# Kernel optimization log

Measured on AMD Instinct MI355X. Metric: run time of the kernel, lower is better.

The kernel has to match this reference:

```python
import jax, jax.numpy as jnp
import numpy as np

SEQ, NSTEPS = 8192, 2048
IDIM, HDIM, NL = 256, 1024, 4


def setup_inputs() -> dict:
    key = jax.random.key(0)
    ks = jax.random.split(key, 6)
    s = 0.02  # small init so tanh recurrence stays well-conditioned
    return {
        "xs": jax.random.normal(ks[0], (SEQ, IDIM), dtype=jnp.float32),
        "Wx0": jax.random.normal(ks[1], (IDIM, HDIM), dtype=jnp.float32) * s,
        "Wh0": jax.random.normal(ks[2], (HDIM, HDIM), dtype=jnp.float32) * s,
        "b0": jnp.zeros((HDIM,), dtype=jnp.float32),
        "Wx_rest": jax.random.normal(ks[3], (NL - 1, HDIM, HDIM), dtype=jnp.float32) * s,
        "Wh_rest": jax.random.normal(ks[4], (NL - 1, HDIM, HDIM), dtype=jnp.float32) * s,
        "b_rest": jnp.zeros((NL - 1, HDIM), dtype=jnp.float32),
        "out_W": jax.random.normal(ks[5], (IDIM, HDIM), dtype=jnp.float32) * s,  # eqx Linear: (out, in)
        "out_b": jnp.zeros((IDIM,), dtype=jnp.float32),
        "n_steps": NSTEPS,
    }


def _layer_scan(xs, Wx, Wh, b):
    # open-loop scan of one tanh RNN cell over the whole sequence
    pre = xs @ Wx + b  # (T, H): hoist input projection out of the scan

    def step(h, p):
        h = jnp.tanh(p + h @ Wh)
        return h, h

    h0 = jnp.zeros((Wh.shape[0],), dtype=xs.dtype)
    last, outs = jax.lax.scan(step, h0, pre)
    return last, outs


def reference(xs, Wx0, Wh0, b0, Wx_rest, Wh_rest, b_rest, out_W, out_b, n_steps):
    # open_loop: run each layer's scan over the full sequence
    states = []
    h, seq = _layer_scan(xs, Wx0, Wh0, b0)
    states.append(h)
    for i in range(Wx_rest.shape[0]):
        h, seq = _layer_scan(seq, Wx_rest[i], Wh_rest[i], b_rest[i])
        states.append(h)
    ol_outs = seq @ out_W.T + out_b  # (T, IDIM) vmap'd out_layer

    def ar_step(carry, _):
        sts, x = carry
        new_sts = []
        h = jnp.tanh(x @ Wx0 + sts[0] @ Wh0 + b0)
        new_sts.append(h)
        x = h
        for i in range(Wx_rest.shape[0]):
            h = jnp.tanh(x @ Wx_rest[i] + sts[i + 1] @ Wh_rest[i] + b_rest[i])
            new_sts.append(h)
            x = h
        x = out_W @ x + out_b
        return (tuple(new_sts), x), x

    carry = (tuple(states), ol_outs[-1])
    _, ar_outs = jax.lax.scan(ar_step, carry, None, length=n_steps)
    return jnp.concatenate([ol_outs, ar_outs], axis=0)  # (T + n_steps, IDIM)
```

## Files before the change

### kernel.cpp

```cpp
#include <hip/hip_runtime.h>
#include <math.h>

#define SEQ    8192
#define NSTEPS 2048
#define NTOT   (SEQ + NSTEPS)
#define IDIM   256
#define HDIM   1024

#define NWG    128
#define TPB    512
#define WPB    8
#define RD     32
#define CREDIT (RD - 8)

typedef unsigned long long u64;

#define WT_FLOATS   (8ull*HDIM*HDIM)
#define BF_FLOAT    WT_FLOATS
#define RING_FLOAT  (WT_FLOATS + HDIM)
#define RING_U64S   (4ull*RD*HDIM)
#define PROG_FLOAT  (RING_FLOAT + 2ull*RING_U64S)


__global__ void k_fuse_w(const float* __restrict__ outW, const float* __restrict__ Wx0,
                         float* __restrict__ ws) {
    int l = blockIdx.x * 256 + threadIdx.x;
    int j = blockIdx.y;
    float acc = 0.f;
    for (int k = 0; k < IDIM; ++k)
        acc += outW[(size_t)k * HDIM + l] * Wx0[(size_t)k * HDIM + j];
    ws[(size_t)j * HDIM + l] = acc;
}

__global__ void k_fuse_b(const float* __restrict__ b0, const float* __restrict__ outb,
                         const float* __restrict__ Wx0, float* __restrict__ ws) {
    int j = blockIdx.x * 256 + threadIdx.x;
    float acc = b0[j];
    for (int k = 0; k < IDIM; ++k)
        acc += outb[k] * Wx0[(size_t)k * HDIM + j];
    ws[BF_FLOAT + j] = acc;
}

__global__ void k_pack(const float* __restrict__ Wh0, const float* __restrict__ Wxr,
                       const float* __restrict__ Whr, float* __restrict__ ws) {
    __shared__ float t[32][33];
    int z = blockIdx.z;
    const float* src; int slot;
    if (z == 0)      { src = Wh0;                                  slot = 1; }
    else if (z <= 3) { src = Wxr + (size_t)(z - 1) * HDIM * HDIM;  slot = 2 * z; }
    else             { src = Whr + (size_t)(z - 4) * HDIM * HDIM;  slot = 2 * (z - 4) + 3; }
    int j0 = blockIdx.x * 32, l0 = blockIdx.y * 32;
    t[threadIdx.y][threadIdx.x] = src[(size_t)(l0 + threadIdx.y) * HDIM + j0 + threadIdx.x];
    __syncthreads();
    float* dst = ws + (size_t)slot * HDIM * HDIM;
    dst[(size_t)(j0 + threadIdx.y) * HDIM + (l0 + threadIdx.x)] = t[threadIdx.x][threadIdx.y];
}

__global__ void k_init(float* __restrict__ ws) {
    int t = blockIdx.x * blockDim.x + threadIdx.x;
    ((u64*)(ws + RING_FLOAT))[t] = 0ull;
    if (t < NWG) ((unsigned*)(ws + PROG_FLOAT))[t] = 0u;
}


__device__ __forceinline__ float wsum(float v) {
#pragma unroll
    for (int off = 32; off > 0; off >>= 1) v += __shfl_xor(v, off, 64);
    return v;
}

__device__ __forceinline__ int wmin(int v) {
#pragma unroll
    for (int off = 32; off > 0; off >>= 1) {
        int o = __shfl_xor(v, off, 64);
        v = o < v ? o : v;
    }
    return v;
}

__device__ __forceinline__ float ftanh(float x) {
    x = fminf(15.f, fmaxf(-15.f, x));
    float e = __builtin_amdgcn_exp2f(x * 2.8853900817779268f);
    return (e - 1.f) * __builtin_amdgcn_rcpf(e + 1.f);
}

__device__ __forceinline__ void capture8(const u64* slot, unsigned want,
                                         float* dst, int lane, int kbase) {
    unsigned done = 0;
    for (;;) {
        u64 v[8];
#pragma unroll
        for (int k = 0; k < 8; ++k) {
            v[k] = 0;
            if (!(done & (1u << k)))
                v[k] = __hip_atomic_load(slot + lane + 64 * (kbase + k),
                                         __ATOMIC_RELAXED, __HIP_MEMORY_SCOPE_AGENT);
        }
#pragma unroll
        for (int k = 0; k < 8; ++k) {
            if (!(done & (1u << k)) && ((unsigned)(v[k] >> 32) == want)) {
                dst[lane + 64 * (kbase + k)] = __uint_as_float((unsigned)v[k]);
                done |= 1u << k;
            }
        }
        if (__all(done == 0xFFu)) return;
    }
}

__global__ __launch_bounds__(TPB, 1) void k_scan(
    const float* __restrict__ xs, const float* __restrict__ Wx0,
    const float* __restrict__ b0, const float* __restrict__ brest,
    const float* __restrict__ outW, const float* __restrict__ outb,
    float* __restrict__ ws, float* __restrict__ out)
{
    const int lane  = threadIdx.x & 63;
    const int wv    = threadIdx.x >> 6;
    const int layer = blockIdx.x >> 5;
    const int wgl   = blockIdx.x & 31;
    const int jw    = wgl * WPB + wv;
    const int j0    = jw * 4;

    __shared__ float ldsOwn[2][HDIM];
    __shared__ float ldsUp[2][HDIM];
    __shared__ int   ldsMinp;

    u64* ring = (u64*)(ws + RING_FLOAT);
    unsigned* prog = (unsigned*)(ws + PROG_FLOAT);
    const int cons = (layer + 1) & 3;

    if (threadIdx.x == 0) ldsMinp = 0;

    float A[4][16], B[4][16];
#pragma unroll
    for (int c = 0; c < 4; ++c)
#pragma unroll
        for (int k = 0; k < 16; ++k) {
            A[c][k] = ws[((size_t)(2 * layer) * HDIM + (j0 + c)) * HDIM + lane + 64 * k];
            B[c][k] = ws[((size_t)(2 * layer + 1) * HDIM + (j0 + c)) * HDIM + lane + 64 * k];
        }
    float wx0[4][4];
    if (layer == 0) {
#pragma unroll
        for (int c = 0; c < 4; ++c)
#pragma unroll
            for (int k = 0; k < 4; ++k)
                wx0[c][k] = Wx0[(size_t)(lane + 64 * k) * HDIM + (j0 + c)];
    }
    float ow[16]; float obv = 0.f;
    if (layer == 3) {
#pragma unroll
        for (int k = 0; k < 16; ++k) ow[k] = outW[(size_t)jw * HDIM + lane + 64 * k];
        obv = outb[jw];
    }
    float bb[4], bfc[4];
#pragma unroll
    for (int c = 0; c < 4; ++c) {
        bb[c]  = (layer == 0) ? b0[j0 + c] : brest[(size_t)(layer - 1) * HDIM + j0 + c];
        bfc[c] = (layer == 0) ? ws[BF_FLOAT + j0 + c] : 0.f;
    }

    float xv[4] = {0.f, 0.f, 0.f, 0.f}, xp[4] = {0.f, 0.f, 0.f, 0.f};
    if (layer == 0) {
#pragma unroll
        for (int k = 0; k < 4; ++k) xv[k] = xs[lane + 64 * k];
    }

    unsigned pvReg = 0;

    __syncthreads();

    for (int n = 1; n <= NTOT; ++n) {
        const int par = n & 1;
        const bool xphase = (layer == 0) && (n <= SEQ);

        if (wv == 5) {
            int m = wmin((int)pvReg);
            if (lane == 0)
                __hip_atomic_store(&ldsMinp, m, __ATOMIC_RELAXED, __HIP_MEMORY_SCOPE_WORKGROUP);
            while (m < n - CREDIT) {
                __builtin_amdgcn_s_sleep(2);
                unsigned p = __hip_atomic_load(&prog[cons * 32 + (lane & 31)],
                                               __ATOMIC_RELAXED, __HIP_MEMORY_SCOPE_AGENT);
                m = wmin((int)p);
                if (lane == 0)
                    __hip_atomic_store(&ldsMinp, m, __ATOMIC_RELAXED, __HIP_MEMORY_SCOPE_WORKGROUP);
            }
        } else {
            if (__hip_atomic_load(&ldsMinp, __ATOMIC_RELAXED, __HIP_MEMORY_SCOPE_WORKGROUP)
                < n - CREDIT) {
                do { __builtin_amdgcn_s_sleep(2); }
                while (__hip_atomic_load(&ldsMinp, __ATOMIC_RELAXED, __HIP_MEMORY_SCOPE_WORKGROUP)
                       < n - CREDIT);
            }
        }

        if (wv < 2) {
            capture8(ring + ((size_t)layer * RD + ((n - 1) & (RD - 1))) * HDIM,
                     (unsigned)(n - 1), ldsOwn[par], lane, wv * 8);
        } else if (wv < 4 && !xphase) {
            const int ul = (layer == 0) ? 3 : layer - 1;
            const unsigned want = (layer == 0) ? (unsigned)(n - 1) : (unsigned)n;
            capture8(ring + ((size_t)ul * RD + (want & (RD - 1))) * HDIM,
                     want, ldsUp[par], lane, (wv - 2) * 8);
        }
        __syncthreads();
        if (threadIdx.x == 0)
            __hip_atomic_store(&prog[blockIdx.x], (unsigned)n, __ATOMIC_RELAXED, __HIP_MEMORY_SCOPE_AGENT);

        if (xphase && n < SEQ) {
            const float* xr = xs + (size_t)n * IDIM;
#pragma unroll
            for (int k = 0; k < 4; ++k) xp[k] = xr[lane + 64 * k];
        }
        if (wv == 5)
            pvReg = __hip_atomic_load(&prog[cons * 32 + (lane & 31)],
                                      __ATOMIC_RELAXED, __HIP_MEMORY_SCOPE_AGENT);

        float a0 = 0.f, a1 = 0.f, a2 = 0.f, a3 = 0.f;
        if (xphase) {
#pragma unroll
            for (int k = 0; k < 4; ++k) {
                float x = xv[k];
                a0 += x * wx0[0][k]; a1 += x * wx0[1][k]; a2 += x * wx0[2][k]; a3 += x * wx0[3][k];
            }
        } else {
#pragma unroll
            for (int k = 0; k < 16; ++k) {
                float x = ldsUp[par][lane + 64 * k];
                a0 += x * A[0][k]; a1 += x * A[1][k]; a2 += x * A[2][k]; a3 += x * A[3][k];
            }
        }
#pragma unroll
        for (int k = 0; k < 16; ++k) {
            float y = ldsOwn[par][lane + 64 * k];
            a0 += y * B[0][k]; a1 += y * B[1][k]; a2 += y * B[2][k]; a3 += y * B[3][k];
        }
        a0 = wsum(a0); a1 = wsum(a1); a2 = wsum(a2); a3 = wsum(a3);
        const bool fph = (layer == 0) && (n > SEQ);
        float r0 = ftanh(a0 + (fph ? bfc[0] : bb[0]));
        float r1 = ftanh(a1 + (fph ? bfc[1] : bb[1]));
        float r2 = ftanh(a2 + (fph ? bfc[2] : bb[2]));
        float r3 = ftanh(a3 + (fph ? bfc[3] : bb[3]));

        {
            u64* dst = ring + ((size_t)layer * RD + (n & (RD - 1))) * HDIM + j0;
            if (lane < 4) {
                float v = (lane == 0) ? r0 : (lane == 1) ? r1 : (lane == 2) ? r2 : r3;
                __hip_atomic_store(dst + lane,
                                   ((u64)(unsigned)n << 32) | (u64)__float_as_uint(v),
                                   __ATOMIC_RELAXED, __HIP_MEMORY_SCOPE_AGENT);
            }
        }

        if (layer == 3 && n >= 2) {
            float a = 0.f;
#pragma unroll
            for (int k = 0; k < 16; ++k) a += ldsOwn[par][lane + 64 * k] * ow[k];
            a = wsum(a);
            if (lane == 0) out[(size_t)(n - 2) * IDIM + jw] = a + obv;
        }

        if (xphase && n < SEQ) {
#pragma unroll
            for (int k = 0; k < 4; ++k) xv[k] = xp[k];
        }
    }

    if (layer == 3) {
        if (wv < 2)
            capture8(ring + ((size_t)3 * RD + (NTOT & (RD - 1))) * HDIM,
                     (unsigned)NTOT, ldsOwn[0], lane, wv * 8);
        __syncthreads();
        float a = 0.f;
#pragma unroll
        for (int k = 0; k < 16; ++k) a += ldsOwn[0][lane + 64 * k] * ow[k];
        a = wsum(a);
        if (lane == 0) out[(size_t)(NTOT - 1) * IDIM + jw] = a + obv;
    }
}


extern "C" void kernel_launch(void* const* d_in, const int* in_sizes, int n_in,
                              void* d_out, int out_size, void* d_ws, size_t ws_size,
                              hipStream_t stream) {
    (void)in_sizes; (void)n_in; (void)out_size; (void)ws_size;
    const float* xs   = (const float*)d_in[0];
    const float* Wx0  = (const float*)d_in[1];
    const float* Wh0  = (const float*)d_in[2];
    const float* b0   = (const float*)d_in[3];
    const float* Wxr  = (const float*)d_in[4];
    const float* Whr  = (const float*)d_in[5];
    const float* brst = (const float*)d_in[6];
    const float* outW = (const float*)d_in[7];
    const float* outb = (const float*)d_in[8];
    float* ws  = (float*)d_ws;
    float* out = (float*)d_out;

    k_fuse_w<<<dim3(4, HDIM), dim3(256), 0, stream>>>(outW, Wx0, ws);
    k_fuse_b<<<dim3(4), dim3(256), 0, stream>>>(b0, outb, Wx0, ws);
    k_pack<<<dim3(32, 32, 7), dim3(32, 32), 0, stream>>>(Wh0, Wxr, Whr, ws);
    k_init<<<dim3(256), dim3(512), 0, stream>>>(ws);

    void* args[] = { (void*)&xs, (void*)&Wx0, (void*)&b0, (void*)&brst,
                     (void*)&outW, (void*)&outb, (void*)&ws, (void*)&out };
    hipError_t e = hipLaunchCooperativeKernel((void*)k_scan, dim3(NWG), dim3(TPB),
                                              args, 0, stream);
    if (e != hipSuccess) {
        k_scan<<<dim3(NWG), dim3(TPB), 0, stream>>>(xs, Wx0, b0, brst, outW, outb, ws, out);
    }
}
```

Baseline: 50.55 ms.

## Halve waves per workgroup, give each wave 8 rows, per-wave credit polling

Each workgroup now has 4 waves instead of 8, and each wave owns 8 hidden rows instead of 4. That doubles the register-resident weights per wave (256 floats for A and B), and each wave now computes two output rows. The shared-LDS credit broadcast from a dedicated wave is replaced by every wave polling the consumer progress flags itself. The capture loop is double-buffered so the next atomic loads are in flight while the previous batch is checked. The aim is to cut per-step barrier and wave-coordination overhead. The cost is much higher register pressure, with possible spills, and more global polling traffic.

```diff
diff --git a/kernel.cpp b/kernel.cpp
--- a/kernel.cpp
+++ b/kernel.cpp
@@ -8,8 +8,8 @@
 #define HDIM   1024
 
 #define NWG    128
-#define TPB    512
-#define WPB    8
+#define TPB    256
+#define WPB    4
 #define RD     32
 #define CREDIT (RD - 8)
 
@@ -86,20 +86,38 @@
 
 __device__ __forceinline__ void capture8(const u64* slot, unsigned want,
                                          float* dst, int lane, int kbase) {
+    const u64* p = slot + lane + 64 * kbase;
     unsigned done = 0;
+    u64 va[8];
+#pragma unroll
+    for (int k = 0; k < 8; ++k)
+        va[k] = __hip_atomic_load(p + 64 * k, __ATOMIC_RELAXED, __HIP_MEMORY_SCOPE_AGENT);
     for (;;) {
-        u64 v[8];
+        u64 vb[8];
 #pragma unroll
         for (int k = 0; k < 8; ++k) {
-            v[k] = 0;
+            vb[k] = 0;
             if (!(done & (1u << k)))
-                v[k] = __hip_atomic_load(slot + lane + 64 * (kbase + k),
-                                         __ATOMIC_RELAXED, __HIP_MEMORY_SCOPE_AGENT);
+                vb[k] = __hip_atomic_load(p + 64 * k, __ATOMIC_RELAXED, __HIP_MEMORY_SCOPE_AGENT);
         }
 #pragma unroll
         for (int k = 0; k < 8; ++k) {
-            if (!(done & (1u << k)) && ((unsigned)(v[k] >> 32) == want)) {
-                dst[lane + 64 * (kbase + k)] = __uint_as_float((unsigned)v[k]);
+            if (!(done & (1u << k)) && ((unsigned)(va[k] >> 32) == want)) {
+                dst[lane + 64 * (kbase + k)] = __uint_as_float((unsigned)va[k]);
+                done |= 1u << k;
+            }
+        }
+        if (__all(done == 0xFFu)) return;
+#pragma unroll
+        for (int k = 0; k < 8; ++k) {
+            va[k] = 0;
+            if (!(done & (1u << k)))
+                va[k] = __hip_atomic_load(p + 64 * k, __ATOMIC_RELAXED, __HIP_MEMORY_SCOPE_AGENT);
+        }
+#pragma unroll
+        for (int k = 0; k < 8; ++k) {
+            if (!(done & (1u << k)) && ((unsigned)(vb[k] >> 32) == want)) {
+                dst[lane + 64 * (kbase + k)] = __uint_as_float((unsigned)vb[k]);
                 done |= 1u << k;
             }
         }
@@ -118,43 +136,43 @@
     const int layer = blockIdx.x >> 5;
     const int wgl   = blockIdx.x & 31;
     const int jw    = wgl * WPB + wv;
-    const int j0    = jw * 4;
+    const int j0    = jw * 8;
 
     __shared__ float ldsOwn[2][HDIM];
     __shared__ float ldsUp[2][HDIM];
-    __shared__ int   ldsMinp;
 
     u64* ring = (u64*)(ws + RING_FLOAT);
     unsigned* prog = (unsigned*)(ws + PROG_FLOAT);
     const int cons = (layer + 1) & 3;
 
-    if (threadIdx.x == 0) ldsMinp = 0;
-
-    float A[4][16], B[4][16];
-#pragma unroll
-    for (int c = 0; c < 4; ++c)
+    float A[8][16], B[8][16];
+#pragma unroll
+    for (int c = 0; c < 8; ++c)
 #pragma unroll
         for (int k = 0; k < 16; ++k) {
             A[c][k] = ws[((size_t)(2 * layer) * HDIM + (j0 + c)) * HDIM + lane + 64 * k];
             B[c][k] = ws[((size_t)(2 * layer + 1) * HDIM + (j0 + c)) * HDIM + lane + 64 * k];
         }
-    float wx0[4][4];
+    float wx0[8][4];
     if (layer == 0) {
 #pragma unroll
-        for (int c = 0; c < 4; ++c)
+        for (int c = 0; c < 8; ++c)
 #pragma unroll
             for (int k = 0; k < 4; ++k)
                 wx0[c][k] = Wx0[(size_t)(lane + 64 * k) * HDIM + (j0 + c)];
     }
-    float ow[16]; float obv = 0.f;
+    float ow0[16], ow1[16]; float ob0 = 0.f, ob1 = 0.f;
     if (layer == 3) {
 #pragma unroll
-        for (int k = 0; k < 16; ++k) ow[k] = outW[(size_t)jw * HDIM + lane + 64 * k];
-        obv = outb[jw];
-    }
-    float bb[4], bfc[4];
-#pragma unroll
-    for (int c = 0; c < 4; ++c) {
+        for (int k = 0; k < 16; ++k) {
+            ow0[k] = outW[(size_t)(2 * jw)     * HDIM + lane + 64 * k];
+            ow1[k] = outW[(size_t)(2 * jw + 1) * HDIM + lane + 64 * k];
+        }
+        ob0 = outb[2 * jw]; ob1 = outb[2 * jw + 1];
+    }
+    float bb[8], bfc[8];
+#pragma unroll
+    for (int c = 0; c < 8; ++c) {
         bb[c]  = (layer == 0) ? b0[j0 + c] : brest[(size_t)(layer - 1) * HDIM + j0 + c];
         bfc[c] = (layer == 0) ? ws[BF_FLOAT + j0 + c] : 0.f;
     }
@@ -165,39 +183,26 @@
         for (int k = 0; k < 4; ++k) xv[k] = xs[lane + 64 * k];
     }
 
-    unsigned pvReg = 0;
-
-    __syncthreads();
+    int minp = 0;
 
     for (int n = 1; n <= NTOT; ++n) {
         const int par = n & 1;
         const bool xphase = (layer == 0) && (n <= SEQ);
 
-        if (wv == 5) {
-            int m = wmin((int)pvReg);
-            if (lane == 0)
-                __hip_atomic_store(&ldsMinp, m, __ATOMIC_RELAXED, __HIP_MEMORY_SCOPE_WORKGROUP);
-            while (m < n - CREDIT) {
+        if (minp < n - CREDIT) {
+            for (;;) {
+                unsigned pv = __hip_atomic_load(&prog[cons * 32 + (lane & 31)],
+                                                __ATOMIC_RELAXED, __HIP_MEMORY_SCOPE_AGENT);
+                minp = wmin((int)pv);
+                if (minp >= n - CREDIT) break;
                 __builtin_amdgcn_s_sleep(2);
-                unsigned p = __hip_atomic_load(&prog[cons * 32 + (lane & 31)],
-                                               __ATOMIC_RELAXED, __HIP_MEMORY_SCOPE_AGENT);
-                m = wmin((int)p);
-                if (lane == 0)
-                    __hip_atomic_store(&ldsMinp, m, __ATOMIC_RELAXED, __HIP_MEMORY_SCOPE_WORKGROUP);
-            }
-        } else {
-            if (__hip_atomic_load(&ldsMinp, __ATOMIC_RELAXED, __HIP_MEMORY_SCOPE_WORKGROUP)
-                < n - CREDIT) {
-                do { __builtin_amdgcn_s_sleep(2); }
-                while (__hip_atomic_load(&ldsMinp, __ATOMIC_RELAXED, __HIP_MEMORY_SCOPE_WORKGROUP)
-                       < n - CREDIT);
             }
         }
 
         if (wv < 2) {
             capture8(ring + ((size_t)layer * RD + ((n - 1) & (RD - 1))) * HDIM,
                      (unsigned)(n - 1), ldsOwn[par], lane, wv * 8);
-        } else if (wv < 4 && !xphase) {
+        } else if (!xphase) {
             const int ul = (layer == 0) ? 3 : layer - 1;
             const unsigned want = (layer == 0) ? (unsigned)(n - 1) : (unsigned)n;
             capture8(ring + ((size_t)ul * RD + (want & (RD - 1))) * HDIM,
@@ -212,52 +217,61 @@
 #pragma unroll
             for (int k = 0; k < 4; ++k) xp[k] = xr[lane + 64 * k];
         }
-        if (wv == 5)
-            pvReg = __hip_atomic_load(&prog[cons * 32 + (lane & 31)],
-                                      __ATOMIC_RELAXED, __HIP_MEMORY_SCOPE_AGENT);
-
-        float a0 = 0.f, a1 = 0.f, a2 = 0.f, a3 = 0.f;
+
+        float acc[8];
+#pragma unroll
+        for (int c = 0; c < 8; ++c) acc[c] = 0.f;
         if (xphase) {
 #pragma unroll
             for (int k = 0; k < 4; ++k) {
                 float x = xv[k];
-                a0 += x * wx0[0][k]; a1 += x * wx0[1][k]; a2 += x * wx0[2][k]; a3 += x * wx0[3][k];
+#pragma unroll
+                for (int c = 0; c < 8; ++c) acc[c] += x * wx0[c][k];
             }
         } else {
 #pragma unroll
             for (int k = 0; k < 16; ++k) {
                 float x = ldsUp[par][lane + 64 * k];
-                a0 += x * A[0][k]; a1 += x * A[1][k]; a2 += x * A[2][k]; a3 += x * A[3][k];
+#pragma unroll
+                for (int c = 0; c < 8; ++c) acc[c] += x * A[c][k];
             }
         }
 #pragma unroll
         for (int k = 0; k < 16; ++k) {
             float y = ldsOwn[par][lane + 64 * k];
-            a0 += y * B[0][k]; a1 += y * B[1][k]; a2 += y * B[2][k]; a3 += y * B[3][k];
-        }
-        a0 = wsum(a0); a1 = wsum(a1); a2 = wsum(a2); a3 = wsum(a3);
+#pragma unroll
+            for (int c = 0; c < 8; ++c) acc[c] += y * B[c][k];
+        }
+#pragma unroll
+        for (int c = 0; c < 8; ++c) acc[c] = wsum(acc[c]);
         const bool fph = (layer == 0) && (n > SEQ);
-        float r0 = ftanh(a0 + (fph ? bfc[0] : bb[0]));
-        float r1 = ftanh(a1 + (fph ? bfc[1] : bb[1]));
-        float r2 = ftanh(a2 + (fph ? bfc[2] : bb[2]));
-        float r3 = ftanh(a3 + (fph ? bfc[3] : bb[3]));
+        float r[8];
+#pragma unroll
+        for (int c = 0; c < 8; ++c) r[c] = ftanh(acc[c] + (fph ? bfc[c] : bb[c]));
 
         {
+            float rv = r[0];
+#pragma unroll
+            for (int c = 1; c < 8; ++c) rv = (lane == c) ? r[c] : rv;
             u64* dst = ring + ((size_t)layer * RD + (n & (RD - 1))) * HDIM + j0;
-            if (lane < 4) {
-                float v = (lane == 0) ? r0 : (lane == 1) ? r1 : (lane == 2) ? r2 : r3;
+            if (lane < 8)
                 __hip_atomic_store(dst + lane,
-                                   ((u64)(unsigned)n << 32) | (u64)__float_as_uint(v),
+                                   ((u64)(unsigned)n << 32) | (u64)__float_as_uint(rv),
                                    __ATOMIC_RELAXED, __HIP_MEMORY_SCOPE_AGENT);
-            }
         }
 
         if (layer == 3 && n >= 2) {
-            float a = 0.f;
-#pragma unroll
-            for (int k = 0; k < 16; ++k) a += ldsOwn[par][lane + 64 * k] * ow[k];
-            a = wsum(a);
-            if (lane == 0) out[(size_t)(n - 2) * IDIM + jw] = a + obv;
+            float o0 = 0.f, o1 = 0.f;
+#pragma unroll
+            for (int k = 0; k < 16; ++k) {
+                float y = ldsOwn[par][lane + 64 * k];
+                o0 += y * ow0[k]; o1 += y * ow1[k];
+            }
+            o0 = wsum(o0); o1 = wsum(o1);
+            if (lane == 0) {
+                out[(size_t)(n - 2) * IDIM + 2 * jw]     = o0 + ob0;
+                out[(size_t)(n - 2) * IDIM + 2 * jw + 1] = o1 + ob1;
+            }
         }
 
         if (xphase && n < SEQ) {
@@ -271,11 +285,17 @@
             capture8(ring + ((size_t)3 * RD + (NTOT & (RD - 1))) * HDIM,
                      (unsigned)NTOT, ldsOwn[0], lane, wv * 8);
         __syncthreads();
-        float a = 0.f;
-#pragma unroll
-        for (int k = 0; k < 16; ++k) a += ldsOwn[0][lane + 64 * k] * ow[k];
-        a = wsum(a);
-        if (lane == 0) out[(size_t)(NTOT - 1) * IDIM + jw] = a + obv;
+        float o0 = 0.f, o1 = 0.f;
+#pragma unroll
+        for (int k = 0; k < 16; ++k) {
+            float y = ldsOwn[0][lane + 64 * k];
+            o0 += y * ow0[k]; o1 += y * ow1[k];
+        }
+        o0 = wsum(o0); o1 = wsum(o1);
+        if (lane == 0) {
+            out[(size_t)(NTOT - 1) * IDIM + 2 * jw]     = o0 + ob0;
+            out[(size_t)(NTOT - 1) * IDIM + 2 * jw + 1] = o1 + ob1;
+        }
     }
 }
 
```

Result: slower. 74.43 ms (+47.2%).
